# Performance work log

Hardware: AMD Instinct MI355X
Metric: run time of the kernel (lower is better)

## Reference

```python
import jax, jax.numpy as jnp
import numpy as np

N = 50000
E = 1600000
IN_C = 128
HEADS = 8
OUT_C = 16
NEG_SLOPE = 0.2  # PyG GATConv default negative_slope


def setup_inputs() -> dict:
    key = jax.random.key(0)
    k1, k2, k3, k4, k5, k6, k7 = jax.random.split(key, 7)
    x = jax.random.normal(k1, (N, IN_C), dtype=jnp.float32)
    x_0 = jax.random.normal(k2, (N, IN_C), dtype=jnp.float32)
    edge_index = jax.random.randint(k3, (2, E), 0, N, dtype=jnp.int64)
    # learned parameters (glorot-ish scale)
    W = jax.random.normal(k4, (IN_C, HEADS * OUT_C), dtype=jnp.float32) * (1.0 / np.sqrt(IN_C))
    att_src = jax.random.normal(k5, (HEADS, OUT_C), dtype=jnp.float32) * (1.0 / np.sqrt(OUT_C))
    att_dst = jax.random.normal(k6, (HEADS, OUT_C), dtype=jnp.float32) * (1.0 / np.sqrt(OUT_C))
    bias = jax.random.normal(k7, (HEADS * OUT_C,), dtype=jnp.float32) * 0.01
    return {"x": x, "x_0": x_0, "W": W, "att_src": att_src,
            "att_dst": att_dst, "bias": bias, "edge_index": edge_index}


def _gat_forward(x, W, att_src, att_dst, bias, edge_index):
    src, dst = edge_index[0], edge_index[1]
    # per-head linear projection: [N, H, C]
    h = (x @ W).reshape(N, HEADS, OUT_C)
    # node-level attention terms: [N, H]
    a_src = jnp.einsum('nhc,hc->nh', h, att_src)
    a_dst = jnp.einsum('nhc,hc->nh', h, att_dst)
    # edge logits + LeakyReLU: [E, H]
    e = jax.nn.leaky_relu(a_src[src] + a_dst[dst], NEG_SLOPE)
    # segment softmax over edges grouped by destination node
    m = jax.ops.segment_max(e, dst, num_segments=N)          # [N, H], -inf for empty
    m = jnp.where(jnp.isfinite(m), m, 0.0)
    ex = jnp.exp(e - m[dst])                                  # [E, H]
    denom = jax.ops.segment_sum(ex, dst, num_segments=N)     # [N, H]
    alpha = ex / (denom[dst] + 1e-16)                         # [E, H]
    # weighted scatter-add aggregation: [N, H, C]
    msg = alpha[:, :, None] * h[src]
    out = jax.ops.segment_sum(msg, dst, num_segments=N)
    out = out.reshape(N, HEADS * OUT_C) + bias                # concat heads + bias
    return jax.nn.relu(out)                                   # unlinear: act='relu'


def reference(x, x_0, W, att_src, att_dst, bias, edge_index):
    # x_0 is accepted by the module's forward but unused
    return _gat_forward(x, W, att_src, att_dst, bias, edge_index)
```

## Files before the change

### kernel.cpp

```cpp
#include <hip/hip_runtime.h>
#include <hip/hip_fp16.h>
#include <math.h>

#define N_NODES 50000
#define E_EDGES 1600000
#define IN_C 128
#define HC 128
#define NEG_SLOPE 0.2f
#define PAD 16
#define NB 391

__global__ __launch_bounds__(256, 2)
void gemm_attn_kernel(const float* __restrict__ x, const float* __restrict__ W,
                      const float* __restrict__ att_src, const float* __restrict__ att_dst,
                      __half* __restrict__ h, float* __restrict__ a_src,
                      float* __restrict__ a_dst)
{
    __shared__ float Ws[128 * 128];
    __shared__ float xs[32 * 128];

    const int tid = threadIdx.x;
    const int c4  = tid & 31;
    const int rg  = tid >> 5;

    for (int i = tid; i < 128 * 128 / 4; i += 256)
        ((float4*)Ws)[i] = ((const float4*)W)[i];

    const float4 asv = ((const float4*)att_src)[c4];
    const float4 adv = ((const float4*)att_dst)[c4];
    const int head = c4 >> 2;

    const float4* Ws4 = (const float4*)Ws;
    const float4* xs4 = (const float4*)xs;

    for (int tile = blockIdx.x; tile * 32 < N_NODES; tile += gridDim.x) {
        const int row_base = tile * 32;
        for (int i = tid; i < 32 * 128 / 4; i += 256) {
            const int r  = i >> 5;
            const int gr = row_base + r;
            float4 v = make_float4(0.f, 0.f, 0.f, 0.f);
            if (gr < N_NODES) v = ((const float4*)x)[gr * 32 + (i & 31)];
            ((float4*)xs)[i] = v;
        }
        __syncthreads();

        float4 acc[4];
        #pragma unroll
        for (int r = 0; r < 4; ++r) acc[r] = make_float4(0.f, 0.f, 0.f, 0.f);

        #pragma unroll 4
        for (int k4 = 0; k4 < 32; ++k4) {
            const float4 w0 = Ws4[(4 * k4 + 0) * 32 + c4];
            const float4 w1 = Ws4[(4 * k4 + 1) * 32 + c4];
            const float4 w2 = Ws4[(4 * k4 + 2) * 32 + c4];
            const float4 w3 = Ws4[(4 * k4 + 3) * 32 + c4];
            #pragma unroll
            for (int r = 0; r < 4; ++r) {
                const float4 xv = xs4[(rg * 4 + r) * 32 + k4];
                acc[r].x = fmaf(xv.x, w0.x, acc[r].x);
                acc[r].y = fmaf(xv.x, w0.y, acc[r].y);
                acc[r].z = fmaf(xv.x, w0.z, acc[r].z);
                acc[r].w = fmaf(xv.x, w0.w, acc[r].w);
                acc[r].x = fmaf(xv.y, w1.x, acc[r].x);
                acc[r].y = fmaf(xv.y, w1.y, acc[r].y);
                acc[r].z = fmaf(xv.y, w1.z, acc[r].z);
                acc[r].w = fmaf(xv.y, w1.w, acc[r].w);
                acc[r].x = fmaf(xv.z, w2.x, acc[r].x);
                acc[r].y = fmaf(xv.z, w2.y, acc[r].y);
                acc[r].z = fmaf(xv.z, w2.z, acc[r].z);
                acc[r].w = fmaf(xv.z, w2.w, acc[r].w);
                acc[r].x = fmaf(xv.w, w3.x, acc[r].x);
                acc[r].y = fmaf(xv.w, w3.y, acc[r].y);
                acc[r].z = fmaf(xv.w, w3.z, acc[r].z);
                acc[r].w = fmaf(xv.w, w3.w, acc[r].w);
            }
        }

        #pragma unroll
        for (int r = 0; r < 4; ++r) {
            const int row = row_base + rg * 4 + r;
            if (row < N_NODES) {
                const __half2 p0 = __floats2half2_rn(acc[r].x, acc[r].y);
                const __half2 p1 = __floats2half2_rn(acc[r].z, acc[r].w);
                uint2 pk;
                pk.x = *(const unsigned int*)&p0;
                pk.y = *(const unsigned int*)&p1;
                ((uint2*)h)[row * 32 + c4] = pk;

                float ps = acc[r].x * asv.x + acc[r].y * asv.y +
                           acc[r].z * asv.z + acc[r].w * asv.w;
                float pd = acc[r].x * adv.x + acc[r].y * adv.y +
                           acc[r].z * adv.z + acc[r].w * adv.w;
                ps += __shfl_xor(ps, 1, 64); ps += __shfl_xor(ps, 2, 64);
                pd += __shfl_xor(pd, 1, 64); pd += __shfl_xor(pd, 2, 64);
                if ((c4 & 3) == 0) {
                    a_src[row * 8 + head] = ps;
                    a_dst[row * 8 + head] = pd;
                }
            }
        }
        __syncthreads();
    }
}

__global__ __launch_bounds__(256)
void cntA_kernel(const int* __restrict__ ei, int* __restrict__ gcnt)
{
    __shared__ int lcnt[NB];
    for (int i = threadIdx.x; i < NB; i += 256) lcnt[i] = 0;
    __syncthreads();
    for (int i = blockIdx.x * 256 + threadIdx.x; i < E_EDGES;
         i += gridDim.x * 256) {
        atomicAdd(&lcnt[ei[E_EDGES + i] >> 7], 1);
    }
    __syncthreads();
    for (int i = threadIdx.x; i < NB; i += 256)
        if (lcnt[i] > 0) atomicAdd(&gcnt[i * PAD], lcnt[i]);
}

__global__ __launch_bounds__(512)
void scanB_kernel(const int* __restrict__ gcnt, int* __restrict__ base,
                  int* __restrict__ cursor)
{
    __shared__ int s[512];
    const int t = threadIdx.x;
    const int v = (t < NB) ? gcnt[t * PAD] : 0;
    s[t] = v;
    __syncthreads();
    #pragma unroll
    for (int d = 1; d < 512; d <<= 1) {
        int x = (t >= d) ? s[t - d] : 0;
        __syncthreads();
        s[t] += x;
        __syncthreads();
    }
    if (t < NB) {
        const int e = s[t] - v;
        base[t] = e;
        cursor[t * PAD] = e;
    }
    if (t == NB - 1) base[NB] = s[t];
}

__global__ __launch_bounds__(256)
void splitA_kernel(const int* __restrict__ ei, int* __restrict__ cursor,
                   unsigned int* __restrict__ bpairs)
{
    const int base_e = (blockIdx.x * 256 + threadIdx.x) * 8;
    if (base_e >= E_EDGES) return;
    int s[8], d[8], pos[8];
    #pragma unroll
    for (int u = 0; u < 8; ++u) s[u] = ei[base_e + u];
    #pragma unroll
    for (int u = 0; u < 8; ++u) d[u] = ei[E_EDGES + base_e + u];
    #pragma unroll
    for (int u = 0; u < 8; ++u) pos[u] = atomicAdd(&cursor[(d[u] >> 7) * PAD], 1);
    #pragma unroll
    for (int u = 0; u < 8; ++u)
        bpairs[pos[u]] = ((unsigned)d[u] << 16) | (unsigned)s[u];
}

__global__ __launch_bounds__(256)
void phaseB_kernel(const int* __restrict__ base,
                   const unsigned int* __restrict__ bpairs,
                   int* __restrict__ csr, int* __restrict__ offs,
                   int* __restrict__ oend)
{
    const int b  = blockIdx.x;
    const int lo = base[b];
    const int hi = base[b + 1];
    const int node0 = b << 7;
    const int t = threadIdx.x;

    __shared__ int cnt[128], loff[128], cur[128];
    if (t < 128) cnt[t] = 0;
    __syncthreads();

    for (int i = lo + t; i < hi; i += 256) {
        const int ld = (int)(bpairs[i] >> 16) - node0;
        atomicAdd(&cnt[ld], 1);
    }
    __syncthreads();

    if (t < 128) loff[t] = cnt[t];
    __syncthreads();
    #pragma unroll
    for (int d = 1; d < 128; d <<= 1) {
        int x = (t >= d && t < 128) ? loff[t - d] : 0;
        __syncthreads();
        if (t < 128) loff[t] += x;
        __syncthreads();
    }
    if (t < 128) {
        const int e = loff[t] - cnt[t];
        cur[t] = e;
        const int node = node0 + t;
        if (node < N_NODES) {
            offs[node] = lo + e;
            oend[node] = lo + e + cnt[t];
        }
    }
    __syncthreads();

    for (int i = lo + t; i < hi; i += 256) {
        const unsigned p = bpairs[i];
        const int ld = (int)(p >> 16) - node0;
        const int pos = lo + atomicAdd(&cur[ld], 1);
        csr[pos] = (int)(p & 0xFFFFu);
    }
}

__global__ __launch_bounds__(256)
void aggregate_kernel(const int* __restrict__ offs, const int* __restrict__ oend,
                      const int* __restrict__ csr_src,
                      const __half* __restrict__ h, const float* __restrict__ a_src,
                      const float* __restrict__ a_dst, const float* __restrict__ bias,
                      float* __restrict__ out)
{
    const int node = blockIdx.x * 4 + (threadIdx.x >> 6);
    if (node >= N_NODES) return;
    const int lane = threadIdx.x & 63;
    const int head = lane >> 3;

    const int start = offs[node];
    const int end   = oend[node];
    const float ad  = a_dst[node * 8 + head];
    const __half2* __restrict__ h2 = (const __half2*)h;

    float accx = 0.f, accy = 0.f, den = 0.f;
    int j = start;
    for (; j + 8 <= end; j += 8) {
        int s[8];
        #pragma unroll
        for (int u = 0; u < 8; ++u) s[u] = csr_src[j + u];
        float lg[8];
        #pragma unroll
        for (int u = 0; u < 8; ++u) lg[u] = a_src[s[u] * 8 + head] + ad;
        __half2 hv[8];
        #pragma unroll
        for (int u = 0; u < 8; ++u) hv[u] = h2[s[u] * 64 + lane];
        #pragma unroll
        for (int u = 0; u < 8; ++u) {
            const float e  = (lg[u] > 0.f) ? lg[u] : lg[u] * NEG_SLOPE;
            const float ex = __expf(e);
            const float2 f = __half22float2(hv[u]);
            accx = fmaf(ex, f.x, accx);
            accy = fmaf(ex, f.y, accy);
            den += ex;
        }
    }
    for (; j < end; ++j) {
        const int src = csr_src[j];
        const float logit = a_src[src * 8 + head] + ad;
        const float e  = (logit > 0.f) ? logit : logit * NEG_SLOPE;
        const float ex = __expf(e);
        const float2 f = __half22float2(h2[src * 64 + lane]);
        accx = fmaf(ex, f.x, accx);
        accy = fmaf(ex, f.y, accy);
        den += ex;
    }
    const float inv = 1.0f / (den + 1e-16f);
    const float2 b = ((const float2*)bias)[lane];
    float2 res;
    res.x = fmaxf(fmaf(accx, inv, b.x), 0.f);
    res.y = fmaxf(fmaf(accy, inv, b.y), 0.f);
    ((float2*)out)[node * 64 + lane] = res;
}

extern "C" void kernel_launch(void* const* d_in, const int* in_sizes, int n_in,
                              void* d_out, int out_size, void* d_ws, size_t ws_size,
                              hipStream_t stream)
{
    const float* x       = (const float*)d_in[0];
    const float* W       = (const float*)d_in[2];
    const float* att_src = (const float*)d_in[3];
    const float* att_dst = (const float*)d_in[4];
    const float* bias    = (const float*)d_in[5];
    const int*   ei      = (const int*)d_in[6];

    float* out = (float*)d_out;

    __half* h     = (__half*)d_ws;
    float* a_src  = (float*)(h + (size_t)N_NODES * HC);
    float* a_dst  = a_src + (size_t)N_NODES * 8;
    int*   offs   = (int*)(a_dst + (size_t)N_NODES * 8);
    int*   oend   = offs + N_NODES;
    int*   gcnt   = oend + N_NODES;
    int*   base   = gcnt + NB * PAD;
    int*   cursor = base + (NB + 1);
    unsigned int* bpairs = (unsigned int*)(cursor + NB * PAD);
    int*   csr    = (int*)(bpairs + E_EDGES);

    hipLaunchKernelGGL(gemm_attn_kernel, dim3(512), dim3(256), 0, stream,
                       x, W, att_src, att_dst, h, a_src, a_dst);

    hipMemsetAsync(gcnt, 0, (size_t)NB * PAD * sizeof(int), stream);
    hipLaunchKernelGGL(cntA_kernel, dim3(256), dim3(256), 0, stream, ei, gcnt);
    hipLaunchKernelGGL(scanB_kernel, dim3(1), dim3(512), 0, stream,
                       gcnt, base, cursor);
    hipLaunchKernelGGL(splitA_kernel, dim3((E_EDGES / 8 + 255) / 256), dim3(256),
                       0, stream, ei, cursor, bpairs);
    hipLaunchKernelGGL(phaseB_kernel, dim3(NB), dim3(256), 0, stream,
                       base, bpairs, csr, offs, oend);

    hipLaunchKernelGGL(aggregate_kernel, dim3((N_NODES + 3) / 4), dim3(256), 0,
                       stream, offs, oend, csr, h, a_src, a_dst, bias, out);
}
```

Measured before the change: 318.9 us.

## Stage bucket scatter in shared memory with per-block local histogram

The edge-bucketing kernel now processes 8192-edge chunks per block. It builds a local histogram of destination buckets in shared memory, scans it, reserves one global range per bucket with a single atomic, stages packed pairs in LDS, then writes them out coalesced. This replaces one global atomic per edge and scattered 4-byte writes with far fewer atomics and contiguous runs per bucket. In exchange it uses about 40KB of LDS per block, only about 196 blocks, and a binary search per output element.

Result: faster. 277.9 us (-12.9%).

```diff
diff --git a/kernel.cpp b/kernel.cpp
--- a/kernel.cpp
+++ b/kernel.cpp
@@ -9,6 +9,8 @@
 #define NEG_SLOPE 0.2f
 #define PAD 16
 #define NB 391
+#define CHUNK 8192
+#define KPT 32
 
 __global__ __launch_bounds__(256, 2)
 void gemm_attn_kernel(const float* __restrict__ x, const float* __restrict__ W,
@@ -146,18 +148,72 @@
 void splitA_kernel(const int* __restrict__ ei, int* __restrict__ cursor,
                    unsigned int* __restrict__ bpairs)
 {
-    const int base_e = (blockIdx.x * 256 + threadIdx.x) * 8;
-    if (base_e >= E_EDGES) return;
-    int s[8], d[8], pos[8];
+    __shared__ int scan[512];
+    __shared__ int loff[NB];
+    __shared__ int lcur[NB];
+    __shared__ int gbase[NB];
+    __shared__ unsigned int stage[CHUNK];
+
+    const int t = threadIdx.x;
+    const int cbase = blockIdx.x * CHUNK;
+
+    for (int i = t; i < 512; i += 256) scan[i] = 0;
+    __syncthreads();
+
+    int dreg[KPT];
     #pragma unroll
-    for (int u = 0; u < 8; ++u) s[u] = ei[base_e + u];
+    for (int k = 0; k < KPT; ++k) {
+        const int i = cbase + k * 256 + t;
+        int d = -1;
+        if (i < E_EDGES) {
+            d = ei[E_EDGES + i];
+            atomicAdd(&scan[d >> 7], 1);
+        }
+        dreg[k] = d;
+    }
+    __syncthreads();
+
+    for (int d = 1; d < 512; d <<= 1) {
+        const int x0 = (t >= d) ? scan[t - d] : 0;
+        const int x1 = scan[t + 256 - d];
+        __syncthreads();
+        scan[t] += x0;
+        scan[t + 256] += x1;
+        __syncthreads();
+    }
+
+    for (int b = t; b < NB; b += 256) {
+        const int inc = scan[b];
+        const int exc = b ? scan[b - 1] : 0;
+        const int c = inc - exc;
+        loff[b] = exc;
+        lcur[b] = 0;
+        if (c > 0) gbase[b] = atomicAdd(&cursor[b * PAD], c);
+    }
+    __syncthreads();
+
     #pragma unroll
-    for (int u = 0; u < 8; ++u) d[u] = ei[E_EDGES + base_e + u];
-    #pragma unroll
-    for (int u = 0; u < 8; ++u) pos[u] = atomicAdd(&cursor[(d[u] >> 7) * PAD], 1);
-    #pragma unroll
-    for (int u = 0; u < 8; ++u)
-        bpairs[pos[u]] = ((unsigned)d[u] << 16) | (unsigned)s[u];
+    for (int k = 0; k < KPT; ++k) {
+        const int i = cbase + k * 256 + t;
+        if (i < E_EDGES) {
+            const int s = ei[i];
+            const int d = dreg[k];
+            const int b = d >> 7;
+            const int l = atomicAdd(&lcur[b], 1);
+            stage[loff[b] + l] = ((unsigned)d << 16) | (unsigned)s;
+        }
+    }
+    __syncthreads();
+
+    const int total = scan[NB - 1];
+    for (int i = t; i < total; i += 256) {
+        int lo = 0, hi = NB - 1;
+        while (lo < hi) {
+            const int mid = (lo + hi + 1) >> 1;
+            if (loff[mid] <= i) lo = mid; else hi = mid - 1;
+        }
+        bpairs[gbase[lo] + (i - loff[lo])] = stage[i];
+    }
 }
 
 __global__ __launch_bounds__(256)
@@ -298,8 +354,8 @@
     hipLaunchKernelGGL(cntA_kernel, dim3(256), dim3(256), 0, stream, ei, gcnt);
     hipLaunchKernelGGL(scanB_kernel, dim3(1), dim3(512), 0, stream,
                        gcnt, base, cursor);
-    hipLaunchKernelGGL(splitA_kernel, dim3((E_EDGES / 8 + 255) / 256), dim3(256),
-                       0, stream, ei, cursor, bpairs);
+    hipLaunchKernelGGL(splitA_kernel, dim3((E_EDGES + CHUNK - 1) / CHUNK),
+                       dim3(256), 0, stream, ei, cursor, bpairs);
     hipLaunchKernelGGL(phaseB_kernel, dim3(NB), dim3(256), 0, stream,
                        base, bpairs, csr, offs, oend);
 
```
